# Kernel optimization log

Measured on AMD Instinct MI355X. Metric: run time of the kernel, lower is better.

## Reference

```python
import jax, jax.numpy as jnp
import numpy as np

CODEBOOK_SIZE = 8192
TOKEN_SIZE = 256
COMMITMENT_COST = 0.25
B, C, H, W = 32, 256, 32, 32


def setup_inputs() -> dict:
    key = jax.random.key(0)
    k1, k2 = jax.random.split(key)
    z = jax.random.normal(k1, (B, C, H, W), dtype=jnp.float32)
    # torch init: uniform_(-1/codebook_size, 1/codebook_size)
    embedding = jax.random.uniform(
        k2, (CODEBOOK_SIZE, TOKEN_SIZE), dtype=jnp.float32,
        minval=-1.0 / CODEBOOK_SIZE, maxval=1.0 / CODEBOOK_SIZE)
    return {"z": z, "embedding": embedding}


def reference(z, embedding):
    # b c h w -> b h w c
    z = jnp.transpose(z.astype(jnp.float32), (0, 2, 3, 1))
    b, h, w, c = z.shape
    z_flat = z.reshape(-1, c)  # [N, c]

    # squared euclidean distances: ||z||^2 + ||e||^2 - 2 z e^T
    d = (jnp.sum(z_flat ** 2, axis=1, keepdims=True)
         + jnp.sum(embedding ** 2, axis=1)
         - 2.0 * jnp.einsum('nd,kd->nk', z_flat, embedding))  # [N, K]
    idx = jnp.argmin(d, axis=1)  # [N]

    z_q = embedding[idx].reshape(z.shape)  # [b,h,w,c]

    commitment_loss = COMMITMENT_COST * jnp.mean(
        (jax.lax.stop_gradient(z_q) - z) ** 2)
    codebook_loss = jnp.mean((z_q - jax.lax.stop_gradient(z)) ** 2)
    loss = commitment_loss + codebook_loss

    # straight-through estimator
    z_q_st = z + jax.lax.stop_gradient(z_q - z)
    z_q_out = jnp.transpose(z_q_st, (0, 3, 1, 2))  # b h w c -> b c h w

    min_encoding_indices = idx.reshape(b, h, w)
    return (z_q_out, loss, commitment_loss, codebook_loss,
            min_encoding_indices)
```

## Files before the change

### kernel.cpp

```cpp
#include <hip/hip_runtime.h>
#include <float.h>

#define NBATCH 32
#define NCHAN  256
#define NHW    1024
#define NTOK   32768
#define NK     8192
#define ND     256
#define ZELEMS 8388608
#define OUT_LOSS 8388608
#define OUT_IDX  8388611
#define MARGIN   1.2e-4f

typedef short bf16x8  __attribute__((ext_vector_type(8)));
typedef float f32x4   __attribute__((ext_vector_type(4)));
typedef float f32x16  __attribute__((ext_vector_type(16)));

__device__ __forceinline__ unsigned short f2bf(float f) {
    unsigned int u = __float_as_uint(f);
    u += 0x7FFFu + ((u >> 16) & 1u);
    return (unsigned short)(u >> 16);
}

__device__ __forceinline__ float embed8(float x, int code) {
    return __int_as_float((__float_as_int(x) & 0xFFFFFF00) | code);
}


__global__ __launch_bounds__(256) void k_cast(const float* __restrict__ zg,
                                              const float* __restrict__ E,
                                              unsigned short* __restrict__ Epre,
                                              unsigned short* __restrict__ Zpre,
                                              float* __restrict__ en,
                                              float* __restrict__ acc,
                                              int* __restrict__ counter) {
    __shared__ unsigned short buf[128][34];
    const int t = threadIdx.x;
    if (blockIdx.x < 1024) {
        int g = blockIdx.x * 256 + t;
        int code = g >> 5, c16 = g & 31;
        int kc = c16 >> 2, ks = (c16 >> 1) & 1, lhi = c16 & 1;
        const float4* E4 = (const float4*)(E + code * ND + c16 * 8);
        float4 a = E4[0], b = E4[1];
        float s = a.x*a.x + a.y*a.y + a.z*a.z + a.w*a.w
                + b.x*b.x + b.y*b.y + b.z*b.z + b.w*b.w;
        #pragma unroll
        for (int off = 1; off < 32; off <<= 1) s += __shfl_xor(s, off, 64);
        if ((t & 31) == 0) en[code] = s;
        unsigned int u[4];
        u[0] = (unsigned int)f2bf(a.x) | ((unsigned int)f2bf(a.y) << 16);
        u[1] = (unsigned int)f2bf(a.z) | ((unsigned int)f2bf(a.w) << 16);
        u[2] = (unsigned int)f2bf(b.x) | ((unsigned int)f2bf(b.y) << 16);
        u[3] = (unsigned int)f2bf(b.z) | ((unsigned int)f2bf(b.w) << 16);
        *(uint4*)((char*)Epre + (size_t)(code >> 7) * 65536 + kc * 8192
                  + (ks * 2 + lhi) * 2048 + (code & 127) * 16) =
            make_uint4(u[0], u[1], u[2], u[3]);
        if (blockIdx.x == 0 && t == 0) { acc[0] = 0.0f; counter[0] = 0; }
    } else {
        int bi = blockIdx.x - 1024;
        int b = bi >> 6, kc = (bi >> 3) & 7, hwt = bi & 7;
        int c0 = kc * 32, hw0 = hwt * 128;
        #pragma unroll
        for (int r = 0; r < 4; ++r) {
            int idx = r * 256 + t;
            int c = idx >> 5, q = idx & 31;
            float4 v = *(const float4*)&zg[(b * 256 + c0 + c) * 1024 + hw0 + q * 4];
            buf[q * 4 + 0][c] = f2bf(v.x);
            buf[q * 4 + 1][c] = f2bf(v.y);
            buf[q * 4 + 2][c] = f2bf(v.z);
            buf[q * 4 + 3][c] = f2bf(v.w);
        }
        __syncthreads();
        int tok = t >> 1, ks = t & 1;
        char* base = (char*)Zpre + (size_t)((b * 8 + hwt) * 8 + kc) * 8192;
        #pragma unroll
        for (int lhi = 0; lhi < 2; ++lhi) {
            unsigned int u[4];
            #pragma unroll
            for (int k = 0; k < 4; ++k) {
                int cc = ks * 16 + lhi * 8 + 2 * k;
                u[k] = (unsigned int)buf[tok][cc] | ((unsigned int)buf[tok][cc + 1] << 16);
            }
            *(uint4*)(base + (ks * 2 + lhi) * 2048 + tok * 16) =
                make_uint4(u[0], u[1], u[2], u[3]);
        }
    }
}

__global__ __launch_bounds__(256, 2) void k_dist(const unsigned short* __restrict__ Epre,
                                                 const unsigned short* __restrict__ Zpre,
                                                 const float* __restrict__ en,
                                                 float2* __restrict__ part2) {
    __shared__ __align__(16) char Elds[3][16384];
    __shared__ __align__(16) char Zlds[3][8192];
    __shared__ float2 red[2][128];
    __shared__ float en_s[256];

    const int t    = threadIdx.x;
    const int kbb2 = blockIdx.x;
    const int mb   = blockIdx.y;
    const int n0   = mb * 128;
    const int w    = t >> 6, lane = t & 63;
    const int l31  = lane & 31, lhi = lane >> 5;
    const int wm   = w >> 1, wn = w & 1;

    const char* Esrc = (const char*)Epre + (size_t)kbb2 * 131072;
    const char* Zsrc = (const char*)Zpre + (size_t)mb * 65536;

    auto STAGE = [&](int bb, int kc) {
        #pragma unroll
        for (int s = 0; s < 2; ++s)
            #pragma unroll
            for (int h = 0; h < 2; ++h)
                __builtin_amdgcn_global_load_lds(
                    (const unsigned int*)(Esrc + (size_t)s * 65536 + kc * 8192 + h * 4096 + t * 16),
                    (unsigned int*)&Elds[bb][s * 8192 + h * 4096 + t * 16], 16, 0, 0);
        #pragma unroll
        for (int h = 0; h < 2; ++h)
            __builtin_amdgcn_global_load_lds(
                (const unsigned int*)(Zsrc + kc * 8192 + h * 4096 + t * 16),
                (unsigned int*)&Zlds[bb][h * 4096 + t * 16], 16, 0, 0);
    };

    bf16x8 eaR[2][4], zbR[2][2];
    const int ebase = wm * 8192 + lhi * 2048 + l31 * 16;
    const int zbase = lhi * 2048 + (wn * 64 + l31) * 16;
    auto LOADSLICE = [&](int set, int bb, int ks) {
        const char* Eb = &Elds[bb][0] + ebase + ks * 4096;
        const char* Zb = &Zlds[bb][0] + zbase + ks * 4096;
        #pragma unroll
        for (int i = 0; i < 4; ++i) eaR[set][i] = *(const bf16x8*)(Eb + i * 512);
        #pragma unroll
        for (int j = 0; j < 2; ++j) zbR[set][j] = *(const bf16x8*)(Zb + j * 512);
    };

    f32x16 acc[4][2];
    #pragma unroll
    for (int i = 0; i < 4; ++i)
        #pragma unroll
        for (int j = 0; j < 2; ++j) acc[i][j] = (f32x16)0.0f;

    __builtin_amdgcn_global_load_lds((const unsigned int*)(en + kbb2 * 256 + t),
                                     (unsigned int*)&en_s[t], 4, 0, 0);
    STAGE(0, 0);
    STAGE(1, 1);
    asm volatile("s_waitcnt vmcnt(6)" ::: "memory");
    __builtin_amdgcn_s_barrier();
    LOADSLICE(0, 0, 0);

    #pragma unroll
    for (int s = 0; s < 16; ++s) {
        const int kc = s >> 1;
        const int cs = s & 1, ns = cs ^ 1;
        if ((s & 1) && kc < 6) STAGE((kc + 2) % 3, kc + 2);
        if ((s & 1) && s < 15) {
            if (s <= 11) { asm volatile("s_waitcnt vmcnt(6)" ::: "memory"); }
            else         { asm volatile("s_waitcnt vmcnt(0)" ::: "memory"); }
            asm volatile("s_waitcnt lgkmcnt(0)" ::: "memory");
            __builtin_amdgcn_s_barrier();
        }
        if (s < 15) LOADSLICE(ns, ((s + 1) >> 1) % 3, (s + 1) & 1);
        __builtin_amdgcn_s_setprio(1);
        #pragma unroll
        for (int i = 0; i < 4; ++i)
            #pragma unroll
            for (int j = 0; j < 2; ++j)
                acc[i][j] = __builtin_amdgcn_mfma_f32_32x32x16_bf16(
                    eaR[cs][i], zbR[cs][j], acc[i][j], 0, 0, 0);
        __builtin_amdgcn_s_setprio(0);
    }

    __syncthreads();

    float v1[2][4], v2[2][4];
    #pragma unroll
    for (int j = 0; j < 2; ++j)
        #pragma unroll
        for (int i = 0; i < 4; ++i) { v1[j][i] = FLT_MAX; v2[j][i] = FLT_MAX; }
    #pragma unroll
    for (int i = 0; i < 4; ++i) {
        const int cb = wm * 128 + i * 32 + lhi * 4;
        #pragma unroll
        for (int rq = 0; rq < 4; ++rq) {
            f32x4 ev = *(const f32x4*)&en_s[cb + 8 * rq];
            #pragma unroll
            for (int rr = 0; rr < 4; ++rr) {
                const int r = rq * 4 + rr;
                const int code = cb + 8 * rq + rr;
                #pragma unroll
                for (int j = 0; j < 2; ++j) {
                    float s  = fmaf(-2.0f, acc[i][j][r], ev[rr]);
                    float se = embed8(s, code);
                    v2[j][i] = __builtin_amdgcn_fmed3f(se, v1[j][i], v2[j][i]);
                    v1[j][i] = fminf(v1[j][i], se);
                }
            }
        }
    }
    float m1[2], m2[2];
    #pragma unroll
    for (int j = 0; j < 2; ++j) {
        float a1 = fminf(v1[j][0], v1[j][1]);
        float ah = fmaxf(v1[j][0], v1[j][1]);
        float a2 = fminf(ah, fminf(v2[j][0], v2[j][1]));
        float b1 = fminf(v1[j][2], v1[j][3]);
        float bh = fmaxf(v1[j][2], v1[j][3]);
        float b2 = fminf(bh, fminf(v2[j][2], v2[j][3]));
        m1[j] = fminf(a1, b1);
        m2[j] = fminf(fmaxf(a1, b1), fminf(a2, b2));
    }
    #pragma unroll
    for (int j = 0; j < 2; ++j) {
        float b1 = __shfl_xor(m1[j], 32, 64);
        float b2 = __shfl_xor(m2[j], 32, 64);
        float hi = fmaxf(m1[j], b1);
        m1[j] = fminf(m1[j], b1);
        m2[j] = fminf(fminf(hi, m2[j]), b2);
    }
    if (lane < 32) {
        #pragma unroll
        for (int j = 0; j < 2; ++j)
            red[wm][wn * 64 + j * 32 + l31] = make_float2(m1[j], m2[j]);
    }
    __syncthreads();
    if (t < 128) {
        float2 A = red[0][t], B = red[1][t];
        float g1 = fminf(A.x, B.x);
        float g2 = fminf(fminf(fmaxf(A.x, B.x), A.y), B.y);
        part2[(size_t)kbb2 * NTOK + n0 + t] = make_float2(g1, g2);
    }
}

__global__ __launch_bounds__(256) void k_refine(const float* __restrict__ zg,
                                                const float* __restrict__ E,
                                                const float2* __restrict__ part2,
                                                int* __restrict__ idxw,
                                                float* __restrict__ outF) {
    __shared__ float Zs[256 * 65];
    const int t = threadIdx.x;
    const int n0 = blockIdx.x * 64;
    const int b = n0 >> 10, hw0 = n0 & 1023;

    #pragma unroll
    for (int r = 0; r < 16; ++r) {
        int li = r * 256 + t;
        int c = li >> 4, q = li & 15;
        float4 v = *(const float4*)&zg[(b * 256 + c) * 1024 + hw0 + q * 4];
        Zs[c * 65 + q * 4 + 0] = v.x;
        Zs[c * 65 + q * 4 + 1] = v.y;
        Zs[c * 65 + q * 4 + 2] = v.z;
        Zs[c * 65 + q * 4 + 3] = v.w;
    }
    __syncthreads();

    const int w = t >> 6, l = t & 63;
    for (int it = 0; it < 16; ++it) {
        const int tokl = w * 16 + it;
        const int n = n0 + tokl;

        float zreg[4];
        #pragma unroll
        for (int j = 0; j < 4; ++j) zreg[j] = Zs[(64 * j + l) * 65 + tokl];

        double z2 = 0.0;
        #pragma unroll
        for (int j = 0; j < 4; ++j) z2 += (double)zreg[j] * (double)zreg[j];
        #pragma unroll
        for (int m = 1; m < 64; m <<= 1) z2 += __shfl_xor(z2, m, 64);
        const float z2f = (float)z2;

        float2 p = make_float2(FLT_MAX, FLT_MAX);
        if (l < 32) p = part2[(size_t)l * NTOK + n];
        int code1 = (l << 8) | (__float_as_int(p.x) & 0xFF);
        int code2 = (l << 8) | (__float_as_int(p.y) & 0xFF);

        float vmin = p.x;
        #pragma unroll
        for (int m = 1; m < 64; m <<= 1) vmin = fminf(vmin, __shfl_xor(vmin, m, 64));
        const float thr = vmin + MARGIN;

        unsigned long long m1 = __ballot(p.x <= thr);
        unsigned long long m2 = __ballot(p.y <= thr);

        float bdq = FLT_MAX; int bidx = 0x7fffffff;
        #pragma unroll
        for (int pass = 0; pass < 2; ++pass) {
            unsigned long long mm = pass ? m2 : m1;
            int ibits = pass ? code2 : code1;
            while (mm) {
                int src = __ffsll(mm) - 1; mm &= mm - 1;
                int cidx = __shfl(ibits, src, 64);
                const float* erow = E + cidx * ND;
                double g = (double)zreg[0] * (double)erow[l]
                         + (double)zreg[1] * (double)erow[64 + l]
                         + (double)zreg[2] * (double)erow[128 + l]
                         + (double)zreg[3] * (double)erow[192 + l];
                #pragma unroll
                for (int mk = 1; mk < 64; mk <<= 1) g += __shfl_xor(g, mk, 64);
                float c  = (float)(2.0 * g);
                float dq = z2f - c;
                if (dq < bdq || (dq == bdq && cidx < bidx)) { bdq = dq; bidx = cidx; }
            }
        }
        if (l == 0) { idxw[n] = bidx; outF[OUT_IDX + n] = (float)bidx; }
    }
}

__global__ __launch_bounds__(256) void k_gather(const float* __restrict__ E,
                                                const float* __restrict__ zg,
                                                const int* __restrict__ idxw,
                                                float* __restrict__ out,
                                                float* __restrict__ acc,
                                                int* __restrict__ counter) {
    __shared__ __align__(16) float Es[64 * 256];
    __shared__ int sidx[64];
    __shared__ float wred[4];
    const int t = threadIdx.x;
    const int b = blockIdx.x >> 4, ht = blockIdx.x & 15;

    if (t < 64) sidx[t] = idxw[b * 1024 + ht * 64 + t];
    __syncthreads();
    const float4* E4 = (const float4*)E;
    #pragma unroll
    for (int r = 0; r < 16; ++r) {
        int li = r * 256 + t;
        int row = li >> 6, slot = li & 63;
        float4 v = E4[(size_t)sidx[row] * 64 + slot];
        *(float4*)&Es[row * 256 + ((slot ^ (row & 15)) * 4)] = v;
    }
    __syncthreads();

    const int hw = t & 63, wv = t >> 6;
    float s = 0.0f;
    #pragma unroll 8
    for (int cc = 0; cc < 64; ++cc) {
        int c = wv * 64 + cc;
        float e = Es[hw * 256 + (((c >> 2) ^ (hw & 15)) * 4) + (c & 3)];
        size_t gi = (size_t)(b * 256 + c) * 1024 + ht * 64 + hw;
        float zv = zg[gi];
        out[gi] = e;
        float d = e - zv;
        s = fmaf(d, d, s);
    }
    #pragma unroll
    for (int off = 32; off > 0; off >>= 1) s += __shfl_down(s, off, 64);
    if ((t & 63) == 0) wred[wv] = s;
    __syncthreads();
    if (t == 0) {
        atomicAdd(acc, wred[0] + wred[1] + wred[2] + wred[3]);
        __threadfence();
        int old = atomicAdd(counter, 1);
        if (old == 511) {
            float total = atomicAdd(acc, 0.0f);
            float mse = total / 8388608.0f;
            out[OUT_LOSS + 0] = 1.25f * mse;
            out[OUT_LOSS + 1] = 0.25f * mse;
            out[OUT_LOSS + 2] = mse;
        }
    }
}

extern "C" void kernel_launch(void* const* d_in, const int* in_sizes, int n_in,
                              void* d_out, int out_size, void* d_ws, size_t ws_size,
                              hipStream_t stream) {
    const float* zg = (const float*)d_in[0];
    const float* E  = (const float*)d_in[1];
    float* out = (float*)d_out;
    float* wsf = (float*)d_ws;
    float*  acc     = wsf;
    int*    counter = (int*)(wsf + 1);
    float*  en      = wsf + 64;
    int*    idxw    = (int*)(wsf + 64 + NK);
    float2* part2   = (float2*)(wsf + 64 + NK + NTOK);
    unsigned short* Epre = (unsigned short*)(wsf + 64 + NK + NTOK + 4194304);
    unsigned short* Zpre = (unsigned short*)d_out;

    k_cast  <<<3072, 256, 0, stream>>>(zg, E, Epre, Zpre, en, acc, counter);
    k_dist  <<<dim3(32, 256), 256, 0, stream>>>(Epre, Zpre, en, part2);
    k_refine<<<NTOK / 64, 256, 0, stream>>>(zg, E, part2, idxw, out);
    k_gather<<<512, 256, 0, stream>>>(E, zg, idxw, out, acc, counter);
}
```

Baseline: 295.9 us.

## Load Z operand directly from global into registers, bypassing LDS staging

The distance GEMM kernel no longer stages the Z tile through shared memory. Each wave now loads its Z fragments straight from global memory into double-buffered registers one chunk ahead, while only the codebook tile still goes through the triple-buffered LDS pipeline. The pipeline is restructured per 32-channel chunk, with new vmcnt thresholds, and the codebook-norm load becomes a plain load plus syncthreads. This cuts LDS traffic and LDS footprint, but increases register pressure and exposes global load latency on the Z operand, which is reloaded redundantly by the two waves sharing the same columns.

```diff
diff --git a/kernel.cpp b/kernel.cpp
--- a/kernel.cpp
+++ b/kernel.cpp
@@ -92,7 +92,6 @@
                                                  const float* __restrict__ en,
                                                  float2* __restrict__ part2) {
     __shared__ __align__(16) char Elds[3][16384];
-    __shared__ __align__(16) char Zlds[3][8192];
     __shared__ float2 red[2][128];
     __shared__ float en_s[256];
 
@@ -107,31 +106,25 @@
     const char* Esrc = (const char*)Epre + (size_t)kbb2 * 131072;
     const char* Zsrc = (const char*)Zpre + (size_t)mb * 65536;
 
-    auto STAGE = [&](int bb, int kc) {
-        #pragma unroll
-        for (int s = 0; s < 2; ++s)
+    auto STAGE_E = [&](int bb, int kc) {
+        #pragma unroll
+        for (int s2 = 0; s2 < 2; ++s2)
             #pragma unroll
             for (int h = 0; h < 2; ++h)
                 __builtin_amdgcn_global_load_lds(
-                    (const unsigned int*)(Esrc + (size_t)s * 65536 + kc * 8192 + h * 4096 + t * 16),
-                    (unsigned int*)&Elds[bb][s * 8192 + h * 4096 + t * 16], 16, 0, 0);
-        #pragma unroll
-        for (int h = 0; h < 2; ++h)
-            __builtin_amdgcn_global_load_lds(
-                (const unsigned int*)(Zsrc + kc * 8192 + h * 4096 + t * 16),
-                (unsigned int*)&Zlds[bb][h * 4096 + t * 16], 16, 0, 0);
+                    (const unsigned int*)(Esrc + (size_t)s2 * 65536 + kc * 8192 + h * 4096 + t * 16),
+                    (unsigned int*)&Elds[bb][s2 * 8192 + h * 4096 + t * 16], 16, 0, 0);
     };
 
-    bf16x8 eaR[2][4], zbR[2][2];
-    const int ebase = wm * 8192 + lhi * 2048 + l31 * 16;
-    const int zbase = lhi * 2048 + (wn * 64 + l31) * 16;
-    auto LOADSLICE = [&](int set, int bb, int ks) {
-        const char* Eb = &Elds[bb][0] + ebase + ks * 4096;
-        const char* Zb = &Zlds[bb][0] + zbase + ks * 4096;
-        #pragma unroll
-        for (int i = 0; i < 4; ++i) eaR[set][i] = *(const bf16x8*)(Eb + i * 512);
-        #pragma unroll
-        for (int j = 0; j < 2; ++j) zbR[set][j] = *(const bf16x8*)(Zb + j * 512);
+    bf16x8 zbR[2][2][2];
+    const char* Zp = Zsrc + lhi * 2048 + (wn * 64 + l31) * 16;
+    auto LOADZ = [&](int set, int kc) {
+        const char* p = Zp + kc * 8192;
+        #pragma unroll
+        for (int j = 0; j < 2; ++j)
+            #pragma unroll
+            for (int ks = 0; ks < 2; ++ks)
+                zbR[set][j][ks] = *(const bf16x8*)(p + ks * 4096 + j * 512);
     };
 
     f32x16 acc[4][2];
@@ -140,33 +133,42 @@
         #pragma unroll
         for (int j = 0; j < 2; ++j) acc[i][j] = (f32x16)0.0f;
 
-    __builtin_amdgcn_global_load_lds((const unsigned int*)(en + kbb2 * 256 + t),
-                                     (unsigned int*)&en_s[t], 4, 0, 0);
-    STAGE(0, 0);
-    STAGE(1, 1);
-    asm volatile("s_waitcnt vmcnt(6)" ::: "memory");
-    __builtin_amdgcn_s_barrier();
-    LOADSLICE(0, 0, 0);
-
-    #pragma unroll
-    for (int s = 0; s < 16; ++s) {
-        const int kc = s >> 1;
-        const int cs = s & 1, ns = cs ^ 1;
-        if ((s & 1) && kc < 6) STAGE((kc + 2) % 3, kc + 2);
-        if ((s & 1) && s < 15) {
-            if (s <= 11) { asm volatile("s_waitcnt vmcnt(6)" ::: "memory"); }
-            else         { asm volatile("s_waitcnt vmcnt(0)" ::: "memory"); }
-            asm volatile("s_waitcnt lgkmcnt(0)" ::: "memory");
+    STAGE_E(0, 0);
+    STAGE_E(1, 1);
+    LOADZ(0, 0);
+    en_s[t] = en[kbb2 * 256 + t];
+    __syncthreads();
+
+    #pragma unroll
+    for (int kc = 0; kc < 8; ++kc) {
+        const int pp = kc & 1, eb = kc % 3;
+        if (kc == 1 || kc == 7) {
+            asm volatile("s_waitcnt vmcnt(8)" ::: "memory");
             __builtin_amdgcn_s_barrier();
-        }
-        if (s < 15) LOADSLICE(ns, ((s + 1) >> 1) % 3, (s + 1) & 1);
+        } else if (kc >= 2) {
+            asm volatile("s_waitcnt vmcnt(12)" ::: "memory");
+            __builtin_amdgcn_s_barrier();
+        }
+        if (kc < 6) STAGE_E((kc + 2) % 3, kc + 2);
+        if (kc < 7) LOADZ(pp ^ 1, kc + 1);
+
+        const char* Eb = &Elds[eb][0] + wm * 8192 + lhi * 2048 + l31 * 16;
+        bf16x8 ea[4][2];
+        #pragma unroll
+        for (int i = 0; i < 4; ++i)
+            #pragma unroll
+            for (int ks = 0; ks < 2; ++ks)
+                ea[i][ks] = *(const bf16x8*)(Eb + ks * 4096 + i * 512);
+
         __builtin_amdgcn_s_setprio(1);
         #pragma unroll
-        for (int i = 0; i < 4; ++i)
-            #pragma unroll
-            for (int j = 0; j < 2; ++j)
-                acc[i][j] = __builtin_amdgcn_mfma_f32_32x32x16_bf16(
-                    eaR[cs][i], zbR[cs][j], acc[i][j], 0, 0, 0);
+        for (int ks = 0; ks < 2; ++ks)
+            #pragma unroll
+            for (int i = 0; i < 4; ++i)
+                #pragma unroll
+                for (int j = 0; j < 2; ++j)
+                    acc[i][j] = __builtin_amdgcn_mfma_f32_32x32x16_bf16(
+                        ea[i][ks], zbR[pp][j][ks], acc[i][j], 0, 0, 0);
         __builtin_amdgcn_s_setprio(0);
     }
 
```

New measurement: 299.9 us. Within noise of the previous version (+1.4%).
